# Kernel optimization log

Measured on AMD Instinct MI355X. Metric: run time of the kernel, lower is better.

Reference implementation:

```python
import jax, jax.numpy as jnp
import numpy as np

B, D, N, H = 1024, 512, 16, 512  # batch, latent, branches, hidden


def _lrelu(v):
    return jnp.where(v >= 0, v, 0.1 * v)  # LeakyReLU(0.1)


def setup_inputs() -> dict:
    key = jax.random.key(0)
    ks = jax.random.split(key, 9)
    s = 0.02
    return {
        "x": jax.random.normal(ks[0], (B, D, N), dtype=jnp.float32),
        "Ws1": jax.random.normal(ks[1], (D, D), dtype=jnp.float32) * s,
        "bs1": jnp.zeros((D,), dtype=jnp.float32),
        "Ws2": jax.random.normal(ks[2], (D, D), dtype=jnp.float32) * s,
        "bs2": jnp.zeros((D,), dtype=jnp.float32),
        # per-branch binary classifiers: Linear(D,H)+LeakyReLU+Linear(H,1)
        "Wc1": jax.random.normal(ks[3], (N, D, H), dtype=jnp.float32) * s,
        "bc1": jnp.zeros((N, H), dtype=jnp.float32),
        "Wc2": jax.random.normal(ks[4], (N, H), dtype=jnp.float32) * s,
        "bc2": jnp.zeros((N,), dtype=jnp.float32),
    }


def reference(x, Ws1, bs1, Ws2, bs2, Wc1, bc1, Wc2, bc2):
    # x: [B, D, N] -> per-branch tokens [B, N, D]
    xb = jnp.transpose(x, (0, 2, 1))
    # shared MLP applied to every branch slice (same weights)
    h = _lrelu(xb @ Ws1 + bs1)
    shared = _lrelu(h @ Ws2 + bs2)  # [B, N, D]
    # per-branch classifier on its own branch slice -> sigmoid probs
    h1 = _lrelu(jnp.einsum('bnd,ndh->bnh', shared, Wc1) + bc1)
    logits = jnp.einsum('bnh,nh->bn', h1, Wc2) + bc2  # [B, N]
    out = jax.nn.sigmoid(logits)[:, None, :]  # [B, 1, N]
    # full pass: concat branch slices along batch (branch-major), every
    # classifier applied to the full stack -> raw logits
    full_in = jnp.transpose(shared, (1, 0, 2)).reshape(N * B, D)  # [M, D]
    h2 = _lrelu(jnp.einsum('md,ndh->mnh', full_in, Wc1) + bc1)  # [M, N, H]
    full_logits = jnp.einsum('mnh,nh->mn', h2, Wc2) + bc2  # [M, N]
    full_out = full_logits[:, None, :]  # [N*B, 1, N]
    return (out, full_out)
```

## Files before the change

kernel.cpp:

```cpp
#include <hip/hip_runtime.h>
#include <hip/hip_bf16.h>
#include <stdint.h>

#define Bq 1024
#define Dq 512
#define Nq 16
#define Hq 512
#define Mq (Bq*Nq)

typedef short v8s  __attribute__((ext_vector_type(8)));
typedef float v4f  __attribute__((ext_vector_type(4)));

typedef __attribute__((address_space(3))) unsigned int as3_u32;
typedef __attribute__((address_space(1))) const unsigned int as1_u32;

__device__ __forceinline__ unsigned short f2bf(float f) {
  union { float f; unsigned u; } v; v.f = f;
  return (unsigned short)((v.u + 0x7fffu + ((v.u >> 16) & 1u)) >> 16);
}

__global__ void k_prep(const float* __restrict__ x,
                       const float* __restrict__ Ws1, const float* __restrict__ Ws2,
                       const float* __restrict__ Wc1,
                       unsigned short* __restrict__ xb,
                       unsigned short* __restrict__ Ws1t, unsigned short* __restrict__ Ws2t,
                       unsigned short* __restrict__ Wc1t) {
  const int bid = blockIdx.x;
  const int t = threadIdx.x;
  if (bid < Bq) {
    __shared__ float lds[Dq][Nq + 1];
    const float* xi = x + (size_t)bid * Dq * Nq;
    for (int p = 0; p < (Dq*Nq)/256; ++p) {
      int i = t + p*256;
      lds[i >> 4][i & (Nq-1)] = xi[i];
    }
    __syncthreads();
    unsigned short* o = xb + (size_t)bid * Nq * Dq;
    for (int p = 0; p < (Dq*Nq)/256; ++p) {
      int i = t + p*256;
      o[i] = f2bf(lds[i & (Dq-1)][i >> 9]);
    }
  } else {
    __shared__ float tile[32][33];
    const int r = bid - Bq;
    const int z = r >> 8;
    const int rem = r & 255;
    const int bx = rem & 15, by = rem >> 4;
    const float* in;
    unsigned short* out;
    if (z == 0)      { in = Ws1; out = Ws1t; }
    else if (z == 1) { in = Ws2; out = Ws2t; }
    else             { in = Wc1 + (size_t)(z-2) * 512 * 512; out = Wc1t + (size_t)(z-2) * 512 * 512; }
    const int tx = t & 31, ty = t >> 5;
    const int c0 = bx * 32, r0 = by * 32;
#pragma unroll
    for (int j = 0; j < 4; ++j)
      tile[ty + j*8][tx] = in[(size_t)(r0 + ty + j*8) * 512 + c0 + tx];
    __syncthreads();
#pragma unroll
    for (int j = 0; j < 4; ++j) {
      int c = c0 + ty + j*8;
      int rr = r0 + tx;
      out[(size_t)c * 512 + rr] = f2bf(tile[tx][ty + j*8]);
    }
  }
}

__global__ __launch_bounds__(256, 2)
void k_gemm2(const unsigned short* __restrict__ A,
             const unsigned short* __restrict__ Bt,
             const float* __restrict__ bias,
             unsigned short* __restrict__ O,
             int permute) {
  __shared__ __align__(16) unsigned short As[2][128][32];
  __shared__ __align__(16) unsigned short Bs[2][256][32];

  const int t = threadIdx.x;
  const int wave = t >> 6, lane = t & 63;
  const int wr = wave >> 1, wc = wave & 1;
  const int fr = lane & 15, fq = lane >> 4;

  const int bm = blockIdx.x * 128;
  const int bn = blockIdx.y * 256;

  const int sr = lane >> 2;
  const int sc = (lane & 3) ^ ((sr >> 1) & 3);
  const unsigned short* aSrc = A  + (size_t)(bm + wave*32 + sr) * Dq + sc*8;
  const unsigned short* bSrc = Bt + (size_t)(bn + wave*64 + sr) * Dq + sc*8;

  auto stage = [&](int buf, int kt) {
#pragma unroll
    for (int j = 0; j < 2; ++j)
      __builtin_amdgcn_global_load_lds((as1_u32*)(aSrc + kt*32 + (size_t)j*16*Dq),
                                       (as3_u32*)&As[buf][wave*32 + j*16][0], 16, 0, 0);
#pragma unroll
    for (int j = 0; j < 4; ++j)
      __builtin_amdgcn_global_load_lds((as1_u32*)(bSrc + kt*32 + (size_t)j*16*Dq),
                                       (as3_u32*)&Bs[buf][wave*64 + j*16][0], 16, 0, 0);
  };

  const int swz = (fq ^ ((fr >> 1) & 3)) * 16;
  int offA[4], offB[8];
#pragma unroll
  for (int mi = 0; mi < 4; ++mi) offA[mi] = (wr*64  + mi*16 + fr) * 64 + swz;
#pragma unroll
  for (int ni = 0; ni < 8; ++ni) offB[ni] = (wc*128 + ni*16 + fr) * 64 + swz;

  v4f acc[4][8] = {};

  stage(0, 0);
  __syncthreads();

  for (int kt = 0; kt < 16; ++kt) {
    const int cur = kt & 1;
    if (kt + 1 < 16) stage(cur ^ 1, kt + 1);

    const char* aB = (const char*)&As[cur][0][0];
    const char* bB = (const char*)&Bs[cur][0][0];
    v8s af[4], bf[8];
#pragma unroll
    for (int mi = 0; mi < 4; ++mi) af[mi] = *(const v8s*)(aB + offA[mi]);
#pragma unroll
    for (int ni = 0; ni < 8; ++ni) bf[ni] = *(const v8s*)(bB + offB[ni]);
#pragma unroll
    for (int mi = 0; mi < 4; ++mi)
#pragma unroll
      for (int ni = 0; ni < 8; ++ni)
        acc[mi][ni] = __builtin_amdgcn_mfma_f32_16x16x32_bf16(af[mi], bf[ni], acc[mi][ni], 0, 0, 0);

    __syncthreads();
  }

  float bcol[8];
#pragma unroll
  for (int ni = 0; ni < 8; ++ni) bcol[ni] = bias[bn + wc*128 + ni*16 + fr];
#pragma unroll
  for (int mi = 0; mi < 4; ++mi) {
#pragma unroll
    for (int reg = 0; reg < 4; ++reg) {
      int grow = bm + wr*64 + mi*16 + fq*4 + reg;
      int orow = permute ? ((grow & 15) * Bq + (grow >> 4)) : grow;
#pragma unroll
      for (int ni = 0; ni < 8; ++ni) {
        int col = bn + wc*128 + ni*16 + fr;
        float v = acc[mi][ni][reg] + bcol[ni];
        v = v >= 0.f ? v : 0.1f * v;
        O[(size_t)orow * 512 + col] = f2bf(v);
      }
    }
  }
}

__global__ __launch_bounds__(256, 2)
void k_headgemm(const unsigned short* __restrict__ A,
                const unsigned short* __restrict__ Bt,
                const float* __restrict__ bias,
                float* __restrict__ FL,
                const float* __restrict__ w2) {
  __shared__ __align__(16) unsigned short As[2][128][32];
  __shared__ __align__(16) unsigned short Bs[2][256][32];

  const int t = threadIdx.x;
  const int wave = t >> 6, lane = t & 63;
  const int wr = wave >> 1, wc = wave & 1;
  const int fr = lane & 15, fq = lane >> 4;

  const int bm = blockIdx.x * 128;
  const int bn = blockIdx.y * 256;
  const int z  = blockIdx.z;

  const unsigned short* Bz = Bt + (size_t)z * Dq * 512;
  const float* biasz = bias + (size_t)z * 512;
  const float* w2z   = w2   + (size_t)z * 512;

  const int sr = lane >> 2;
  const int sc = (lane & 3) ^ ((sr >> 1) & 3);
  const unsigned short* aSrc = A  + (size_t)(bm + wave*32 + sr) * Dq + sc*8;
  const unsigned short* bSrc = Bz + (size_t)(bn + wave*64 + sr) * Dq + sc*8;

  auto stage = [&](int buf, int kt) {
#pragma unroll
    for (int j = 0; j < 2; ++j)
      __builtin_amdgcn_global_load_lds((as1_u32*)(aSrc + kt*32 + (size_t)j*16*Dq),
                                       (as3_u32*)&As[buf][wave*32 + j*16][0], 16, 0, 0);
#pragma unroll
    for (int j = 0; j < 4; ++j)
      __builtin_amdgcn_global_load_lds((as1_u32*)(bSrc + kt*32 + (size_t)j*16*Dq),
                                       (as3_u32*)&Bs[buf][wave*64 + j*16][0], 16, 0, 0);
  };

  const int swz = (fq ^ ((fr >> 1) & 3)) * 16;
  int offA[4], offB[8];
#pragma unroll
  for (int mi = 0; mi < 4; ++mi) offA[mi] = (wr*64  + mi*16 + fr) * 64 + swz;
#pragma unroll
  for (int ni = 0; ni < 8; ++ni) offB[ni] = (wc*128 + ni*16 + fr) * 64 + swz;

  v4f acc[4][8] = {};

  stage(0, 0);
  __syncthreads();

  for (int kt = 0; kt < 16; ++kt) {
    const int cur = kt & 1;
    if (kt + 1 < 16) stage(cur ^ 1, kt + 1);

    const char* aB = (const char*)&As[cur][0][0];
    const char* bB = (const char*)&Bs[cur][0][0];
    v8s af[4], bf[8];
#pragma unroll
    for (int mi = 0; mi < 4; ++mi) af[mi] = *(const v8s*)(aB + offA[mi]);
#pragma unroll
    for (int ni = 0; ni < 8; ++ni) bf[ni] = *(const v8s*)(bB + offB[ni]);
#pragma unroll
    for (int mi = 0; mi < 4; ++mi)
#pragma unroll
      for (int ni = 0; ni < 8; ++ni)
        acc[mi][ni] = __builtin_amdgcn_mfma_f32_16x16x32_bf16(af[mi], bf[ni], acc[mi][ni], 0, 0, 0);

    __syncthreads();
  }

  float bcol[8], wcol[8];
#pragma unroll
  for (int ni = 0; ni < 8; ++ni) {
    int col = bn + wc*128 + ni*16 + fr;
    bcol[ni] = biasz[col];
    wcol[ni] = w2z[col];
  }
#pragma unroll
  for (int mi = 0; mi < 4; ++mi) {
#pragma unroll
    for (int reg = 0; reg < 4; ++reg) {
      float s = 0.f;
#pragma unroll
      for (int ni = 0; ni < 8; ++ni) {
        float v = acc[mi][ni][reg] + bcol[ni];
        v = v >= 0.f ? v : 0.1f * v;
        s += v * wcol[ni];
      }
#pragma unroll
      for (int off = 1; off < 16; off <<= 1)
        s += __shfl_xor(s, off, 64);
      if (fr == 0) {
        int grow = bm + wr*64 + mi*16 + fq*4 + reg;
        atomicAdd(&FL[(size_t)grow * Nq + z], s);
      }
    }
  }
}

__global__ void k_final(const float* __restrict__ fl, const float* __restrict__ bc2,
                        float* __restrict__ out) {
  int i = blockIdx.x * 256 + threadIdx.x;
  int m = i >> 4, n = i & 15;
  float v = fl[i] + bc2[n];
  out[Mq + i] = v;
  if (n == (m >> 10)) {
    int b = m & (Bq - 1);
    out[b * Nq + n] = 1.f / (1.f + __expf(-v));
  }
}

extern "C" void kernel_launch(void* const* d_in, const int* in_sizes, int n_in,
                              void* d_out, int out_size, void* d_ws, size_t ws_size,
                              hipStream_t stream) {
  (void)in_sizes; (void)n_in; (void)out_size; (void)ws_size;
  const float* x   = (const float*)d_in[0];
  const float* Ws1 = (const float*)d_in[1];
  const float* bs1 = (const float*)d_in[2];
  const float* Ws2 = (const float*)d_in[3];
  const float* bs2 = (const float*)d_in[4];
  const float* Wc1 = (const float*)d_in[5];
  const float* bc1 = (const float*)d_in[6];
  const float* Wc2 = (const float*)d_in[7];
  const float* bc2 = (const float*)d_in[8];

  char* ws = (char*)d_ws;
  unsigned short* Xb   = (unsigned short*)(ws);
  unsigned short* Hbuf = (unsigned short*)(ws + (size_t)16*1024*1024);
  unsigned short* Sm   = (unsigned short*)(ws + (size_t)32*1024*1024);
  unsigned short* Ws1t = (unsigned short*)(ws + (size_t)48*1024*1024);
  unsigned short* Ws2t = (unsigned short*)(ws + (size_t)48*1024*1024 + 512*1024);
  unsigned short* Wc1t = (unsigned short*)(ws + (size_t)49*1024*1024);
  float*          FL   = (float*)         (ws + (size_t)57*1024*1024);

  hipMemsetAsync(FL, 0, (size_t)Mq * Nq * sizeof(float), stream);

  k_prep<<<Bq + 18*256, 256, 0, stream>>>(x, Ws1, Ws2, Wc1, Xb, Ws1t, Ws2t, Wc1t);

  k_gemm2<<<dim3(128,2), 256, 0, stream>>>(Xb,   Ws1t, bs1, Hbuf, 0);
  k_gemm2<<<dim3(128,2), 256, 0, stream>>>(Hbuf, Ws2t, bs2, Sm,   1);
  k_headgemm<<<dim3(128,2,16), 256, 0, stream>>>(Sm, Wc1t, bc1, FL, Wc2);

  k_final<<<(Mq*Nq)/256, 256, 0, stream>>>(FL, bc2, (float*)d_out);
}
```

Baseline: 325.7 us.

## Retile head GEMM to 128x128 with BK=64 and split atomic partials

```diff
diff --git a/kernel.cpp b/kernel.cpp
--- a/kernel.cpp
+++ b/kernel.cpp
@@ -155,10 +155,10 @@
 void k_headgemm(const unsigned short* __restrict__ A,
                 const unsigned short* __restrict__ Bt,
                 const float* __restrict__ bias,
-                float* __restrict__ FL,
+                float* __restrict__ FL2,
                 const float* __restrict__ w2) {
-  __shared__ __align__(16) unsigned short As[2][128][32];
-  __shared__ __align__(16) unsigned short Bs[2][256][32];
+  __shared__ __align__(16) unsigned short As[2][128][64];
+  __shared__ __align__(16) unsigned short Bs[2][128][64];
 
   const int t = threadIdx.x;
   const int wave = t >> 6, lane = t & 63;
@@ -166,75 +166,87 @@
   const int fr = lane & 15, fq = lane >> 4;
 
   const int bm = blockIdx.x * 128;
-  const int bn = blockIdx.y * 256;
+  const int bn = blockIdx.y * 128;
   const int z  = blockIdx.z;
 
   const unsigned short* Bz = Bt + (size_t)z * Dq * 512;
   const float* biasz = bias + (size_t)z * 512;
   const float* w2z   = w2   + (size_t)z * 512;
 
-  const int sr = lane >> 2;
-  const int sc = (lane & 3) ^ ((sr >> 1) & 3);
-  const unsigned short* aSrc = A  + (size_t)(bm + wave*32 + sr) * Dq + sc*8;
-  const unsigned short* bSrc = Bz + (size_t)(bn + wave*64 + sr) * Dq + sc*8;
+  const int sr8 = lane >> 3;
+  const int sc8 = (lane & 7) ^ sr8;
+  const unsigned short* aSrc = A  + (size_t)(bm + wave*32 + sr8) * Dq + sc8*8;
+  const unsigned short* bSrc = Bz + (size_t)(bn + wave*32 + sr8) * Dq + sc8*8;
 
   auto stage = [&](int buf, int kt) {
 #pragma unroll
-    for (int j = 0; j < 2; ++j)
-      __builtin_amdgcn_global_load_lds((as1_u32*)(aSrc + kt*32 + (size_t)j*16*Dq),
-                                       (as3_u32*)&As[buf][wave*32 + j*16][0], 16, 0, 0);
-#pragma unroll
-    for (int j = 0; j < 4; ++j)
-      __builtin_amdgcn_global_load_lds((as1_u32*)(bSrc + kt*32 + (size_t)j*16*Dq),
-                                       (as3_u32*)&Bs[buf][wave*64 + j*16][0], 16, 0, 0);
+    for (int g = 0; g < 4; ++g)
+      __builtin_amdgcn_global_load_lds((as1_u32*)(aSrc + kt*64 + (size_t)g*8*Dq),
+                                       (as3_u32*)&As[buf][wave*32 + g*8][0], 16, 0, 0);
+#pragma unroll
+    for (int g = 0; g < 4; ++g)
+      __builtin_amdgcn_global_load_lds((as1_u32*)(bSrc + kt*64 + (size_t)g*8*Dq),
+                                       (as3_u32*)&Bs[buf][wave*32 + g*8][0], 16, 0, 0);
   };
 
-  const int swz = (fq ^ ((fr >> 1) & 3)) * 16;
-  int offA[4], offB[8];
-#pragma unroll
-  for (int mi = 0; mi < 4; ++mi) offA[mi] = (wr*64  + mi*16 + fr) * 64 + swz;
-#pragma unroll
-  for (int ni = 0; ni < 8; ++ni) offB[ni] = (wc*128 + ni*16 + fr) * 64 + swz;
-
-  v4f acc[4][8] = {};
+  int offA[4][2], offB[4][2];
+#pragma unroll
+  for (int mi = 0; mi < 4; ++mi) {
+    int r = wr*64 + mi*16 + fr;
+#pragma unroll
+    for (int kh = 0; kh < 2; ++kh)
+      offA[mi][kh] = r*128 + (((kh*4 + fq) ^ (fr & 7)) * 16);
+  }
+#pragma unroll
+  for (int ni = 0; ni < 4; ++ni) {
+    int r = wc*64 + ni*16 + fr;
+#pragma unroll
+    for (int kh = 0; kh < 2; ++kh)
+      offB[ni][kh] = r*128 + (((kh*4 + fq) ^ (fr & 7)) * 16);
+  }
+
+  v4f acc[4][4] = {};
 
   stage(0, 0);
   __syncthreads();
 
-  for (int kt = 0; kt < 16; ++kt) {
+  for (int kt = 0; kt < 8; ++kt) {
     const int cur = kt & 1;
-    if (kt + 1 < 16) stage(cur ^ 1, kt + 1);
+    if (kt + 1 < 8) stage(cur ^ 1, kt + 1);
 
     const char* aB = (const char*)&As[cur][0][0];
     const char* bB = (const char*)&Bs[cur][0][0];
-    v8s af[4], bf[8];
-#pragma unroll
-    for (int mi = 0; mi < 4; ++mi) af[mi] = *(const v8s*)(aB + offA[mi]);
-#pragma unroll
-    for (int ni = 0; ni < 8; ++ni) bf[ni] = *(const v8s*)(bB + offB[ni]);
-#pragma unroll
-    for (int mi = 0; mi < 4; ++mi)
-#pragma unroll
-      for (int ni = 0; ni < 8; ++ni)
-        acc[mi][ni] = __builtin_amdgcn_mfma_f32_16x16x32_bf16(af[mi], bf[ni], acc[mi][ni], 0, 0, 0);
-
+#pragma unroll
+    for (int kh = 0; kh < 2; ++kh) {
+      v8s af[4], bf[4];
+#pragma unroll
+      for (int mi = 0; mi < 4; ++mi) af[mi] = *(const v8s*)(aB + offA[mi][kh]);
+#pragma unroll
+      for (int ni = 0; ni < 4; ++ni) bf[ni] = *(const v8s*)(bB + offB[ni][kh]);
+#pragma unroll
+      for (int mi = 0; mi < 4; ++mi)
+#pragma unroll
+        for (int ni = 0; ni < 4; ++ni)
+          acc[mi][ni] = __builtin_amdgcn_mfma_f32_16x16x32_bf16(af[mi], bf[ni], acc[mi][ni], 0, 0, 0);
+    }
     __syncthreads();
   }
 
-  float bcol[8], wcol[8];
-#pragma unroll
-  for (int ni = 0; ni < 8; ++ni) {
-    int col = bn + wc*128 + ni*16 + fr;
+  float bcol[4], wcol[4];
+#pragma unroll
+  for (int ni = 0; ni < 4; ++ni) {
+    int col = bn + wc*64 + ni*16 + fr;
     bcol[ni] = biasz[col];
     wcol[ni] = w2z[col];
   }
+  float* FLp = FL2 + (size_t)blockIdx.y * Mq * Nq;
 #pragma unroll
   for (int mi = 0; mi < 4; ++mi) {
 #pragma unroll
     for (int reg = 0; reg < 4; ++reg) {
       float s = 0.f;
 #pragma unroll
-      for (int ni = 0; ni < 8; ++ni) {
+      for (int ni = 0; ni < 4; ++ni) {
         float v = acc[mi][ni][reg] + bcol[ni];
         v = v >= 0.f ? v : 0.1f * v;
         s += v * wcol[ni];
@@ -244,17 +256,18 @@
         s += __shfl_xor(s, off, 64);
       if (fr == 0) {
         int grow = bm + wr*64 + mi*16 + fq*4 + reg;
-        atomicAdd(&FL[(size_t)grow * Nq + z], s);
+        atomicAdd(&FLp[(size_t)grow * Nq + z], s);
       }
     }
   }
 }
 
-__global__ void k_final(const float* __restrict__ fl, const float* __restrict__ bc2,
+__global__ void k_final(const float* __restrict__ fl2, const float* __restrict__ bc2,
                         float* __restrict__ out) {
   int i = blockIdx.x * 256 + threadIdx.x;
   int m = i >> 4, n = i & 15;
-  float v = fl[i] + bc2[n];
+  float v = fl2[i] + fl2[(size_t)Mq*Nq + i] + fl2[2*(size_t)Mq*Nq + i]
+          + fl2[3*(size_t)Mq*Nq + i] + bc2[n];
   out[Mq + i] = v;
   if (n == (m >> 10)) {
     int b = m & (Bq - 1);
@@ -283,15 +296,15 @@
   unsigned short* Ws1t = (unsigned short*)(ws + (size_t)48*1024*1024);
   unsigned short* Ws2t = (unsigned short*)(ws + (size_t)48*1024*1024 + 512*1024);
   unsigned short* Wc1t = (unsigned short*)(ws + (size_t)49*1024*1024);
-  float*          FL   = (float*)         (ws + (size_t)57*1024*1024);
-
-  hipMemsetAsync(FL, 0, (size_t)Mq * Nq * sizeof(float), stream);
+  float*          FL2  = (float*)         (ws + (size_t)57*1024*1024);
+
+  hipMemsetAsync(FL2, 0, (size_t)4 * Mq * Nq * sizeof(float), stream);
 
   k_prep<<<Bq + 18*256, 256, 0, stream>>>(x, Ws1, Ws2, Wc1, Xb, Ws1t, Ws2t, Wc1t);
 
   k_gemm2<<<dim3(128,2), 256, 0, stream>>>(Xb,   Ws1t, bs1, Hbuf, 0);
   k_gemm2<<<dim3(128,2), 256, 0, stream>>>(Hbuf, Ws2t, bs2, Sm,   1);
-  k_headgemm<<<dim3(128,2,16), 256, 0, stream>>>(Sm, Wc1t, bc1, FL, Wc2);
-
-  k_final<<<(Mq*Nq)/256, 256, 0, stream>>>(FL, bc2, (float*)d_out);
-}
+  k_headgemm<<<dim3(128,4,16), 256, 0, stream>>>(Sm, Wc1t, bc1, FL2, Wc2);
+
+  k_final<<<(Mq*Nq)/256, 256, 0, stream>>>(FL2, bc2, (float*)d_out);
+}
```

Result: slower. 379.4 us (+16.5%).
